# Kernel tuning notes

Hardware: AMD Instinct MI355X
Metric: run time of the kernel (lower is better)

Reference implementation:

```python
import jax, jax.numpy as jnp
import numpy as np
from jax import lax

H = 1024
E = 8
TOP_K = 2


def setup_inputs() -> dict:
    key = jax.random.key(0)
    kx, k1, k2 = jax.random.split(key, 3)
    x = jax.random.normal(kx, (8, 2048, H), dtype=jnp.float32)
    # router MLP params, init normal(0, 0.02), zero bias (matches _init_weights)
    w1 = jax.random.normal(k1, (H, 2 * H), dtype=jnp.float32) * 0.02
    b1 = jnp.zeros((2 * H,), dtype=jnp.float32)
    w2 = jax.random.normal(k2, (2 * H, E), dtype=jnp.float32) * 0.02
    b2 = jnp.zeros((E,), dtype=jnp.float32)
    return {"x": x, "w1": w1, "b1": b1, "w2": w2, "b2": b2}


def reference(x, w1, b1, w2, b2):
    # gating MLP: Linear -> GELU (exact, torch default) -> Linear
    h = jax.nn.gelu(jnp.einsum('bsh,hf->bsf', x, w1) + b1, approximate=False)
    expert_weights = jnp.einsum('bsf,fe->bse', h, w2) + b2  # [B,S,E]

    top_k_weights, top_k_indices = lax.top_k(expert_weights, TOP_K)  # [B,S,K]
    top_k_weights = jax.nn.softmax(top_k_weights, axis=-1)

    # scatter renormalized weights into dense [B,S,E] mask (indices distinct -> one-hot sum)
    onehot = jax.nn.one_hot(top_k_indices, E, dtype=expert_weights.dtype)  # [B,S,K,E]
    masks = jnp.einsum('bsk,bske->bse', top_k_weights, onehot)

    expert_usage = masks.sum(axis=(0, 1))
    expert_usage = expert_usage / expert_usage.sum()
    target_usage = jnp.full_like(expert_usage, 1.0 / E)
    load_balancing_loss = jnp.mean((expert_usage - target_usage) ** 2)

    sparsity_loss = jnp.mean(jnp.sum(masks > 0, axis=-1).astype(jnp.float32)) / TOP_K
    total_loss = load_balancing_loss + 0.1 * sparsity_loss

    return expert_weights, masks, total_loss, expert_usage
```

## Files before the change

### kernel.cpp

```cpp
#include <hip/hip_runtime.h>
#include <math.h>

#define HDIM 1024
#define FDIM 2048
#define NEXP 8
#define MTOK 16384
#define NSLC 32


typedef __attribute__((ext_vector_type(8))) short bf16x8;
typedef __attribute__((ext_vector_type(16))) float f32x16;

__device__ inline unsigned short f2bf_rne(float f) {
    unsigned int u = __float_as_uint(f);
    u = (u + 0x7FFFu + ((u >> 16) & 1u)) >> 16;
    return (unsigned short)u;
}
__device__ inline float bf2f(unsigned short h) {
    unsigned int u = ((unsigned int)h) << 16;
    return __uint_as_float(u);
}

__global__ __launch_bounds__(256) void cvt_x(const float* __restrict__ x,
                                             unsigned short* __restrict__ af)
{
    __shared__ unsigned short hs[16384];
    __shared__ unsigned short ls[16384];
    const int mt = blockIdx.x;
    const int m = threadIdx.x & 31;
    const int kc = threadIdx.x >> 5;
    const float* src = x + ((size_t)mt * 32 + m) * HDIM;
    unsigned short* dst = af + (size_t)mt * 65536;

    #pragma unroll
    for (int p = 0; p < 2; p++) {
        #pragma unroll
        for (int i = 0; i < 8; i++) {
            int k_local = kc * 64 + i * 8;
            int k = p * 512 + k_local;
            float v[8];
            *(float4*)(v)     = *(const float4*)(src + k);
            *(float4*)(v + 4) = *(const float4*)(src + k + 4);
            union { unsigned short u[8]; uint4 q; } oh, ol;
            #pragma unroll
            for (int j = 0; j < 8; j++) {
                unsigned short h = f2bf_rne(v[j]);
                oh.u[j] = h;
                ol.u[j] = f2bf_rne(v[j] - bf2f(h));
            }
            int ks_l = k_local >> 4;
            int lane = ((k_local >> 3) & 1) * 32 + m;
            int o = ks_l * 512 + lane * 8;
            *(uint4*)(hs + o) = oh.q;
            *(uint4*)(ls + o) = ol.q;
        }
        __syncthreads();
        unsigned short* dp = dst + p * 32768;
        #pragma unroll
        for (int c = 0; c < 16; c++) {
            int f = c * 2048 + threadIdx.x * 8;
            int ks_l = f >> 10, hl = (f >> 9) & 1, rest = f & 511;
            const unsigned short* s = (hl ? ls : hs) + ks_l * 512 + rest;
            *(uint4*)(dp + f) = *(const uint4*)s;
        }
        __syncthreads();
    }
}

__global__ __launch_bounds__(256) void cvt_w1f(const float* __restrict__ w1,
                                               unsigned short* __restrict__ wf)
{
    __shared__ float t[32][33];
    int n0 = blockIdx.x * 32;
    int k0 = blockIdx.y * 32;
    int lx = threadIdx.x & 31, ly = threadIdx.x >> 5;
    #pragma unroll
    for (int r = 0; r < 32; r += 8)
        t[ly + r][lx] = w1[(size_t)(k0 + ly + r) * FDIM + n0 + lx];
    __syncthreads();
    #pragma unroll
    for (int r = 0; r < 32; r += 8) {
        float v = t[lx][ly + r];
        unsigned short h = f2bf_rne(v);
        unsigned short l = f2bf_rne(v - bf2f(h));
        int n = n0 + ly + r, k = k0 + lx;
        size_t base = ((size_t)(n >> 5) * 64 + (k >> 4)) * 1024;
        int lj = (((k >> 3) & 1) * 32 + (n & 31)) * 8 + (k & 7);
        wf[base + lj] = h;
        wf[base + 512 + lj] = l;
    }
}

__global__ __launch_bounds__(256, 3) void gemm1_mfma(
    const unsigned short* __restrict__ af, const unsigned short* __restrict__ wf,
    const float* __restrict__ b1, const float* __restrict__ w2,
    float* __restrict__ part)
{
    const int tid  = threadIdx.x;
    const int lane = tid & 63;
    const int l31  = lane & 31;
    const int half = lane >> 5;
    const int wave = tid >> 6;
    const int wm   = wave & 1;
    const int wn   = wave >> 1;

    const int id = blockIdx.x;
    const int xcd = id & 7, seq = id >> 3;
    const int strip = seq >> 6;
    const int bn = (seq >> 2) & 15;
    const int bmo = seq & 3;
    const int bm = strip * 32 + xcd * 4 + bmo;
    const int m0 = bm * 128, n0 = bn * 128;

    const unsigned short* ap[2];
    const unsigned short* bp[2];
    #pragma unroll
    for (int i = 0; i < 2; i++)
        ap[i] = af + (size_t)(bm * 4 + wm * 2 + i) * 65536 + lane * 8;
    #pragma unroll
    for (int j = 0; j < 2; j++)
        bp[j] = wf + (size_t)(bn * 4 + wn * 2 + j) * 65536 + lane * 8;

    f32x16 acc[2][2];
    #pragma unroll
    for (int i = 0; i < 2; i++)
        #pragma unroll
        for (int j = 0; j < 2; j++)
            #pragma unroll
            for (int r = 0; r < 16; r++) acc[i][j][r] = 0.f;

    bf16x8 Ah0[2], Al0[2], Bh0[2], Bl0[2];
    bf16x8 Ah1[2], Al1[2], Bh1[2], Bl1[2];

    #pragma unroll
    for (int i = 0; i < 2; i++) {
        Ah0[i] = *(const bf16x8*)(ap[i]);
        Al0[i] = *(const bf16x8*)(ap[i] + 512);
        Bh0[i] = *(const bf16x8*)(bp[i]);
        Bl0[i] = *(const bf16x8*)(bp[i] + 512);
    }

    #pragma unroll 1
    for (int t = 0; t < 64; t += 2) {
        #pragma unroll
        for (int i = 0; i < 2; i++) {
            Ah1[i] = *(const bf16x8*)(ap[i] + 1024);
            Al1[i] = *(const bf16x8*)(ap[i] + 1536);
            Bh1[i] = *(const bf16x8*)(bp[i] + 1024);
            Bl1[i] = *(const bf16x8*)(bp[i] + 1536);
        }
        #pragma unroll
        for (int i = 0; i < 2; i++)
            #pragma unroll
            for (int j = 0; j < 2; j++)
                acc[i][j] = __builtin_amdgcn_mfma_f32_32x32x16_bf16(
                    Ah0[i], Bh0[j], acc[i][j], 0, 0, 0);
        #pragma unroll
        for (int i = 0; i < 2; i++)
            #pragma unroll
            for (int j = 0; j < 2; j++)
                acc[i][j] = __builtin_amdgcn_mfma_f32_32x32x16_bf16(
                    Ah0[i], Bl0[j], acc[i][j], 0, 0, 0);
        #pragma unroll
        for (int i = 0; i < 2; i++)
            #pragma unroll
            for (int j = 0; j < 2; j++)
                acc[i][j] = __builtin_amdgcn_mfma_f32_32x32x16_bf16(
                    Al0[i], Bh0[j], acc[i][j], 0, 0, 0);
        #pragma unroll
        for (int i = 0; i < 2; i++) { ap[i] += 2048; bp[i] += 2048; }
        #pragma unroll
        for (int i = 0; i < 2; i++) {
            Ah0[i] = *(const bf16x8*)(ap[i]);
            Al0[i] = *(const bf16x8*)(ap[i] + 512);
            Bh0[i] = *(const bf16x8*)(bp[i]);
            Bl0[i] = *(const bf16x8*)(bp[i] + 512);
        }
        #pragma unroll
        for (int i = 0; i < 2; i++)
            #pragma unroll
            for (int j = 0; j < 2; j++)
                acc[i][j] = __builtin_amdgcn_mfma_f32_32x32x16_bf16(
                    Ah1[i], Bh1[j], acc[i][j], 0, 0, 0);
        #pragma unroll
        for (int i = 0; i < 2; i++)
            #pragma unroll
            for (int j = 0; j < 2; j++)
                acc[i][j] = __builtin_amdgcn_mfma_f32_32x32x16_bf16(
                    Ah1[i], Bl1[j], acc[i][j], 0, 0, 0);
        #pragma unroll
        for (int i = 0; i < 2; i++)
            #pragma unroll
            for (int j = 0; j < 2; j++)
                acc[i][j] = __builtin_amdgcn_mfma_f32_32x32x16_bf16(
                    Al1[i], Bh1[j], acc[i][j], 0, 0, 0);

        #pragma unroll
        for (int g = 0; g < 8; g++) {
            __builtin_amdgcn_sched_group_barrier(0x020, 2, 0);
            __builtin_amdgcn_sched_group_barrier(0x008, 3, 0);
        }
    }

    #pragma unroll
    for (int j = 0; j < 2; j++) {
        int n = n0 + wn * 64 + j * 32 + l31;
        float bb = b1[n];
        #pragma unroll
        for (int i = 0; i < 2; i++)
            #pragma unroll
            for (int r = 0; r < 16; r++) {
                float v = acc[i][j][r] + bb;
                acc[i][j][r] = 0.5f * v * (1.0f + erff(v * 0.70710678118654752f));
            }
    }

    float w2r[2][8];
    #pragma unroll
    for (int j = 0; j < 2; j++) {
        const float4* p = (const float4*)(w2 + (size_t)(n0 + wn * 64 + j * 32 + l31) * NEXP);
        float4 u = p[0], v = p[1];
        w2r[j][0] = u.x; w2r[j][1] = u.y; w2r[j][2] = u.z; w2r[j][3] = u.w;
        w2r[j][4] = v.x; w2r[j][5] = v.y; w2r[j][6] = v.z; w2r[j][7] = v.w;
    }

    const int sl = bn * 2 + wn;
    #pragma unroll
    for (int e = 0; e < NEXP; e++) {
        float p[2][16];
        #pragma unroll
        for (int i = 0; i < 2; i++)
            #pragma unroll
            for (int r = 0; r < 16; r++)
                p[i][r] = acc[i][0][r] * w2r[0][e] + acc[i][1][r] * w2r[1][e];
        #pragma unroll
        for (int off = 1; off < 32; off <<= 1)
            #pragma unroll
            for (int i = 0; i < 2; i++)
                #pragma unroll
                for (int r = 0; r < 16; r++)
                    p[i][r] += __shfl_xor(p[i][r], off);
        if (l31 == 0) {
            #pragma unroll
            for (int i = 0; i < 2; i++)
                #pragma unroll
                for (int r = 0; r < 16; r++) {
                    int m = m0 + wm * 64 + i * 32 + (r & 3) + 8 * (r >> 2) + 4 * half;
                    part[(size_t)sl * (MTOK * NEXP) + (size_t)m * NEXP + e] = p[i][r];
                }
        }
    }
}

__global__ __launch_bounds__(256) void router_topk(
    const float* __restrict__ part, const float* __restrict__ b2,
    float* __restrict__ out, float* __restrict__ gu, int* __restrict__ gc)
{
    const int t = blockIdx.x * 256 + threadIdx.x;

    float logit[8];
    #pragma unroll
    for (int e = 0; e < 8; e++) logit[e] = b2[e];
    #pragma unroll
    for (int j = 0; j < NSLC; j++) {
        const float4* p4 = (const float4*)(part + (size_t)j * (MTOK * NEXP) + (size_t)t * NEXP);
        float4 u = p4[0], v = p4[1];
        logit[0] += u.x; logit[1] += u.y; logit[2] += u.z; logit[3] += u.w;
        logit[4] += v.x; logit[5] += v.y; logit[6] += v.z; logit[7] += v.w;
    }

    int i1 = 0; float v1 = logit[0];
    #pragma unroll
    for (int e = 1; e < 8; e++) { if (logit[e] > v1) { v1 = logit[e]; i1 = e; } }
    int i2 = -1; float v2 = -INFINITY;
    #pragma unroll
    for (int e = 0; e < 8; e++) {
        if (e != i1 && logit[e] > v2) { v2 = logit[e]; i2 = e; }
    }
    float ex = expf(v2 - v1);
    float inv = 1.0f / (1.0f + ex);
    float wa = inv, wb = ex * inv;

    float4* o = (float4*)(out + (size_t)t * NEXP);
    o[0] = make_float4(logit[0], logit[1], logit[2], logit[3]);
    o[1] = make_float4(logit[4], logit[5], logit[6], logit[7]);

    float mk[8];
    #pragma unroll
    for (int e = 0; e < 8; e++) mk[e] = 0.0f;
    mk[i1] = wa; mk[i2] = wb;
    float4* om = (float4*)(out + (size_t)(MTOK * NEXP) + (size_t)t * NEXP);
    om[0] = make_float4(mk[0], mk[1], mk[2], mk[3]);
    om[1] = make_float4(mk[4], mk[5], mk[6], mk[7]);

    __shared__ float us[8];
    __shared__ int cs;
    if (threadIdx.x < 8) us[threadIdx.x] = 0.0f;
    if (threadIdx.x == 0) cs = 0;
    __syncthreads();
    atomicAdd(&us[i1], wa);
    atomicAdd(&us[i2], wb);
    int cnt = (wa > 0.0f ? 1 : 0) + (wb > 0.0f ? 1 : 0);
    atomicAdd(&cs, cnt);
    __syncthreads();
    if (threadIdx.x < 8) atomicAdd(&gu[threadIdx.x], us[threadIdx.x]);
    if (threadIdx.x == 0) atomicAdd(gc, cs);
}

__global__ void router_final(const float* __restrict__ gu, const int* __restrict__ gc,
                             float* __restrict__ out)
{
    if (blockIdx.x == 0 && threadIdx.x == 0) {
        float u[8]; float tot = 0.0f;
        for (int e = 0; e < 8; e++) { u[e] = gu[e]; tot += u[e]; }
        float lb = 0.0f;
        for (int e = 0; e < 8; e++) {
            float un = u[e] / tot;
            out[2 * MTOK * NEXP + 1 + e] = un;
            float d = un - 0.125f;
            lb += d * d;
        }
        lb *= (1.0f / 8.0f);
        float sp = ((float)(*gc) / (float)MTOK) * 0.5f;
        out[2 * MTOK * NEXP] = lb + 0.1f * sp;
    }
}

extern "C" void kernel_launch(void* const* d_in, const int* in_sizes, int n_in,
                              void* d_out, int out_size, void* d_ws, size_t ws_size,
                              hipStream_t stream) {
    const float* x  = (const float*)d_in[0];
    const float* w1 = (const float*)d_in[1];
    const float* b1 = (const float*)d_in[2];
    const float* w2 = (const float*)d_in[3];
    const float* b2 = (const float*)d_in[4];
    float* out = (float*)d_out;

    unsigned short* af = (unsigned short*)d_ws;
    unsigned short* wf = af + (size_t)512 * 65536;
    float* part = (float*)(wf + (size_t)64 * 65536);
    float* gu = part + (size_t)NSLC * MTOK * NEXP;
    int* gc = (int*)(gu + 8);

    hipMemsetAsync(gu, 0, 64, stream);

    cvt_x<<<512, 256, 0, stream>>>(x, af);
    cvt_w1f<<<dim3(FDIM / 32, HDIM / 32), 256, 0, stream>>>(w1, wf);
    gemm1_mfma<<<2048, 256, 0, stream>>>(af, wf, b1, w2, part);
    router_topk<<<MTOK / 256, 256, 0, stream>>>(part, b2, out, gu, gc);
    router_final<<<1, 64, 0, stream>>>(gu, gc, out);
}
```

Baseline: 409.9 us.

## Stage GEMM tiles through double-buffered LDS via global_load_lds and fuse final reduction

Restructures the GEMM main loop so each wave loads one 2048-element slice of A and B straight into double-buffered shared memory with global_load_lds. All four waves then read the operands they need from LDS, instead of each wave loading both its A and B fragments from global memory, which duplicated reads. Occupancy drops to 2 blocks per CU, and a __syncthreads is added every K step. The router_final launch is also folded into router_topk using a last-block atomic counter, which removes one kernel launch.

```diff
diff --git a/kernel.cpp b/kernel.cpp
--- a/kernel.cpp
+++ b/kernel.cpp
@@ -91,11 +91,14 @@
     }
 }
 
-__global__ __launch_bounds__(256, 3) void gemm1_mfma(
+__global__ __launch_bounds__(256, 2) void gemm1_mfma(
     const unsigned short* __restrict__ af, const unsigned short* __restrict__ wf,
     const float* __restrict__ b1, const float* __restrict__ w2,
     float* __restrict__ part)
 {
+    __shared__ __align__(16) short As[2][8192];
+    __shared__ __align__(16) short Bs[2][8192];
+
     const int tid  = threadIdx.x;
     const int lane = tid & 63;
     const int l31  = lane & 31;
@@ -112,93 +115,81 @@
     const int bm = strip * 32 + xcd * 4 + bmo;
     const int m0 = bm * 128, n0 = bn * 128;
 
-    const unsigned short* ap[2];
-    const unsigned short* bp[2];
+    const unsigned short* asrc = af + (size_t)(bm * 4 + wave) * 65536 + lane * 8;
+    const unsigned short* bsrc = wf + (size_t)(bn * 4 + wave) * 65536 + lane * 8;
+
+    f32x16 acc[2][2];
     #pragma unroll
     for (int i = 0; i < 2; i++)
-        ap[i] = af + (size_t)(bm * 4 + wm * 2 + i) * 65536 + lane * 8;
-    #pragma unroll
-    for (int j = 0; j < 2; j++)
-        bp[j] = wf + (size_t)(bn * 4 + wn * 2 + j) * 65536 + lane * 8;
-
-    f32x16 acc[2][2];
-    #pragma unroll
-    for (int i = 0; i < 2; i++)
         #pragma unroll
         for (int j = 0; j < 2; j++)
             #pragma unroll
             for (int r = 0; r < 16; r++) acc[i][j][r] = 0.f;
 
-    bf16x8 Ah0[2], Al0[2], Bh0[2], Bl0[2];
-    bf16x8 Ah1[2], Al1[2], Bh1[2], Bl1[2];
-
-    #pragma unroll
-    for (int i = 0; i < 2; i++) {
-        Ah0[i] = *(const bf16x8*)(ap[i]);
-        Al0[i] = *(const bf16x8*)(ap[i] + 512);
-        Bh0[i] = *(const bf16x8*)(bp[i]);
-        Bl0[i] = *(const bf16x8*)(bp[i] + 512);
+    #pragma unroll
+    for (int c = 0; c < 4; c++) {
+        __builtin_amdgcn_global_load_lds(
+            (const __attribute__((address_space(1))) void*)(asrc + c * 512),
+            (__attribute__((address_space(3))) void*)&As[0][wave * 2048 + c * 512],
+            16, 0, 0);
+        __builtin_amdgcn_global_load_lds(
+            (const __attribute__((address_space(1))) void*)(bsrc + c * 512),
+            (__attribute__((address_space(3))) void*)&Bs[0][wave * 2048 + c * 512],
+            16, 0, 0);
     }
 
     #pragma unroll 1
-    for (int t = 0; t < 64; t += 2) {
-        #pragma unroll
-        for (int i = 0; i < 2; i++) {
-            Ah1[i] = *(const bf16x8*)(ap[i] + 1024);
-            Al1[i] = *(const bf16x8*)(ap[i] + 1536);
-            Bh1[i] = *(const bf16x8*)(bp[i] + 1024);
-            Bl1[i] = *(const bf16x8*)(bp[i] + 1536);
-        }
-        #pragma unroll
-        for (int i = 0; i < 2; i++)
-            #pragma unroll
-            for (int j = 0; j < 2; j++)
-                acc[i][j] = __builtin_amdgcn_mfma_f32_32x32x16_bf16(
-                    Ah0[i], Bh0[j], acc[i][j], 0, 0, 0);
-        #pragma unroll
-        for (int i = 0; i < 2; i++)
-            #pragma unroll
-            for (int j = 0; j < 2; j++)
-                acc[i][j] = __builtin_amdgcn_mfma_f32_32x32x16_bf16(
-                    Ah0[i], Bl0[j], acc[i][j], 0, 0, 0);
-        #pragma unroll
-        for (int i = 0; i < 2; i++)
-            #pragma unroll
-            for (int j = 0; j < 2; j++)
-                acc[i][j] = __builtin_amdgcn_mfma_f32_32x32x16_bf16(
-                    Al0[i], Bh0[j], acc[i][j], 0, 0, 0);
-        #pragma unroll
-        for (int i = 0; i < 2; i++) { ap[i] += 2048; bp[i] += 2048; }
-        #pragma unroll
-        for (int i = 0; i < 2; i++) {
-            Ah0[i] = *(const bf16x8*)(ap[i]);
-            Al0[i] = *(const bf16x8*)(ap[i] + 512);
-            Bh0[i] = *(const bf16x8*)(bp[i]);
-            Bl0[i] = *(const bf16x8*)(bp[i] + 512);
-        }
-        #pragma unroll
-        for (int i = 0; i < 2; i++)
-            #pragma unroll
-            for (int j = 0; j < 2; j++)
-                acc[i][j] = __builtin_amdgcn_mfma_f32_32x32x16_bf16(
-                    Ah1[i], Bh1[j], acc[i][j], 0, 0, 0);
-        #pragma unroll
-        for (int i = 0; i < 2; i++)
-            #pragma unroll
-            for (int j = 0; j < 2; j++)
-                acc[i][j] = __builtin_amdgcn_mfma_f32_32x32x16_bf16(
-                    Ah1[i], Bl1[j], acc[i][j], 0, 0, 0);
-        #pragma unroll
-        for (int i = 0; i < 2; i++)
-            #pragma unroll
-            for (int j = 0; j < 2; j++)
-                acc[i][j] = __builtin_amdgcn_mfma_f32_32x32x16_bf16(
-                    Al1[i], Bh1[j], acc[i][j], 0, 0, 0);
-
-        #pragma unroll
-        for (int g = 0; g < 8; g++) {
-            __builtin_amdgcn_sched_group_barrier(0x020, 2, 0);
-            __builtin_amdgcn_sched_group_barrier(0x008, 3, 0);
+    for (int t = 0; t < 32; t++) {
+        __syncthreads();
+        if (t + 1 < 32) {
+            const int nb = (t + 1) & 1;
+            const unsigned short* an = asrc + (t + 1) * 2048;
+            const unsigned short* bnp = bsrc + (t + 1) * 2048;
+            #pragma unroll
+            for (int c = 0; c < 4; c++) {
+                __builtin_amdgcn_global_load_lds(
+                    (const __attribute__((address_space(1))) void*)(an + c * 512),
+                    (__attribute__((address_space(3))) void*)&As[nb][wave * 2048 + c * 512],
+                    16, 0, 0);
+                __builtin_amdgcn_global_load_lds(
+                    (const __attribute__((address_space(1))) void*)(bnp + c * 512),
+                    (__attribute__((address_space(3))) void*)&Bs[nb][wave * 2048 + c * 512],
+                    16, 0, 0);
+            }
+        }
+        const short* a = As[t & 1];
+        const short* b = Bs[t & 1];
+
+        #pragma unroll
+        for (int s = 0; s < 2; s++) {
+            bf16x8 Ah[2], Al[2], Bh[2], Bl[2];
+            #pragma unroll
+            for (int i = 0; i < 2; i++) {
+                int ao = (2 * wm + i) * 2048 + s * 1024 + lane * 8;
+                Ah[i] = *(const bf16x8*)&a[ao];
+                Al[i] = *(const bf16x8*)&a[ao + 512];
+                int bo = (2 * wn + i) * 2048 + s * 1024 + lane * 8;
+                Bh[i] = *(const bf16x8*)&b[bo];
+                Bl[i] = *(const bf16x8*)&b[bo + 512];
+            }
+            #pragma unroll
+            for (int i = 0; i < 2; i++)
+                #pragma unroll
+                for (int j = 0; j < 2; j++)
+                    acc[i][j] = __builtin_amdgcn_mfma_f32_32x32x16_bf16(
+                        Ah[i], Bh[j], acc[i][j], 0, 0, 0);
+            #pragma unroll
+            for (int i = 0; i < 2; i++)
+                #pragma unroll
+                for (int j = 0; j < 2; j++)
+                    acc[i][j] = __builtin_amdgcn_mfma_f32_32x32x16_bf16(
+                        Ah[i], Bl[j], acc[i][j], 0, 0, 0);
+            #pragma unroll
+            for (int i = 0; i < 2; i++)
+                #pragma unroll
+                for (int j = 0; j < 2; j++)
+                    acc[i][j] = __builtin_amdgcn_mfma_f32_32x32x16_bf16(
+                        Al[i], Bh[j], acc[i][j], 0, 0, 0);
         }
     }
 
@@ -254,7 +245,8 @@
 
 __global__ __launch_bounds__(256) void router_topk(
     const float* __restrict__ part, const float* __restrict__ b2,
-    float* __restrict__ out, float* __restrict__ gu, int* __restrict__ gc)
+    float* __restrict__ out, float* __restrict__ gu, int* __restrict__ gc,
+    int* __restrict__ gd)
 {
     const int t = blockIdx.x * 256 + threadIdx.x;
 
@@ -295,6 +287,7 @@
 
     __shared__ float us[8];
     __shared__ int cs;
+    __shared__ int lastf;
     if (threadIdx.x < 8) us[threadIdx.x] = 0.0f;
     if (threadIdx.x == 0) cs = 0;
     __syncthreads();
@@ -305,15 +298,17 @@
     __syncthreads();
     if (threadIdx.x < 8) atomicAdd(&gu[threadIdx.x], us[threadIdx.x]);
     if (threadIdx.x == 0) atomicAdd(gc, cs);
-}
-
-__global__ void router_final(const float* __restrict__ gu, const int* __restrict__ gc,
-                             float* __restrict__ out)
-{
-    if (blockIdx.x == 0 && threadIdx.x == 0) {
+    __threadfence();
+    if (threadIdx.x == 0)
+        lastf = (atomicAdd(gd, 1) == (int)gridDim.x - 1) ? 1 : 0;
+    __syncthreads();
+    if (lastf && threadIdx.x == 0) {
         float u[8]; float tot = 0.0f;
-        for (int e = 0; e < 8; e++) { u[e] = gu[e]; tot += u[e]; }
+        #pragma unroll
+        for (int e = 0; e < 8; e++) { u[e] = atomicAdd(&gu[e], 0.0f); tot += u[e]; }
+        int c = atomicAdd(gc, 0);
         float lb = 0.0f;
+        #pragma unroll
         for (int e = 0; e < 8; e++) {
             float un = u[e] / tot;
             out[2 * MTOK * NEXP + 1 + e] = un;
@@ -321,7 +316,7 @@
             lb += d * d;
         }
         lb *= (1.0f / 8.0f);
-        float sp = ((float)(*gc) / (float)MTOK) * 0.5f;
+        float sp = ((float)c / (float)MTOK) * 0.5f;
         out[2 * MTOK * NEXP] = lb + 0.1f * sp;
     }
 }
@@ -341,12 +336,12 @@
     float* part = (float*)(wf + (size_t)64 * 65536);
     float* gu = part + (size_t)NSLC * MTOK * NEXP;
     int* gc = (int*)(gu + 8);
+    int* gd = gc + 1;
 
     hipMemsetAsync(gu, 0, 64, stream);
 
     cvt_x<<<512, 256, 0, stream>>>(x, af);
     cvt_w1f<<<dim3(FDIM / 32, HDIM / 32), 256, 0, stream>>>(w1, wf);
     gemm1_mfma<<<2048, 256, 0, stream>>>(af, wf, b1, w2, part);
-    router_topk<<<MTOK / 256, 256, 0, stream>>>(part, b2, out, gu, gc);
-    router_final<<<1, 64, 0, stream>>>(gu, gc, out);
-}
+    router_topk<<<MTOK / 256, 256, 0, stream>>>(part, b2, out, gu, gc, gd);
+}
```

After: 432.3 us. +5.5%, slower.
